# Kernel tuning notes

Measured on AMD Instinct MI355X. Metric: run time of the kernel, lower is better.

## Reference

```python
import jax, jax.numpy as jnp
import numpy as np

ENC_L, DEC_L = 4, 6
H = 8
D = 512
DFF = 2048
DLAT = 128
NTOK = 1024
NCODES = 2048
NGROUPS = 64
DG = DLAT // NGROUPS  # 2
T_ENC, BT, NSEQ = 128, 8, 16
T_DEC = 1024


def sinusoid_pe(T, d):
    pos = jnp.arange(T, dtype=jnp.float32)[:, None]
    div = jnp.exp(jnp.arange(0, d, 2, dtype=jnp.float32) * (-jnp.log(10000.0) / d))
    pe = jnp.zeros((T, d), jnp.float32)
    pe = pe.at[:, 0::2].set(jnp.sin(pos * div))
    pe = pe.at[:, 1::2].set(jnp.cos(pos * div))
    return pe[:, None, :]  # [T,1,d], seq-first broadcast over batch


def layer_norm(x, g, b):
    m = x.mean(-1, keepdims=True)
    v = ((x - m) ** 2).mean(-1, keepdims=True)
    return (x - m) * jax.lax.rsqrt(v + 1e-5) * g + b


def mha(x, Wqkv, Wo, causal):
    T, B, d = x.shape
    dh = d // H
    q, k, v = jnp.split(x @ Wqkv, 3, axis=-1)
    q = q.reshape(T, B, H, dh)
    k = k.reshape(T, B, H, dh)
    v = v.reshape(T, B, H, dh)
    scores = jnp.einsum('tbhd,sbhd->bhts', q, k) / jnp.sqrt(jnp.float32(dh))
    if causal:
        mask = jnp.tril(jnp.ones((T, T), bool))
        scores = jnp.where(mask[None, None], scores, jnp.float32(-1e9))
    attn = jax.nn.softmax(scores, axis=-1)
    out = jnp.einsum('bhts,sbhd->tbhd', attn, v).reshape(T, B, d)
    return out @ Wo


def tf_layer(x, p, i, causal):
    Wqkv, Wo, ln1g, ln1b, ln2g, ln2b, W1, b1, W2, b2 = [a[i] for a in p]
    x = layer_norm(x + mha(x, Wqkv, Wo, causal), ln1g, ln1b)
    h = jax.nn.relu(x @ W1 + b1) @ W2 + b2
    return layer_norm(x + h, ln2g, ln2b)


def forward_core(enc_inp, dec_inp, dec_inp_seq_pos, fl):
    (emb_table,
     eWqkv, eWo, eln1g, eln1b, eln2g, eln2b, eW1, eb1, eW2, eb2,
     dWqkv, dWo, dln1g, dln1b, dln2g, dln2b, dW1, db1, dW2, db2,
     W_mu, b_mu, codebook, seg_W, seg_b, W_out, b_out) = fl
    scale = jnp.sqrt(jnp.float32(D))
    # token embeddings (seq-first)
    enc_emb = emb_table[enc_inp] * scale            # [T_ENC, BT, NSEQ, D]
    dec_emb = emb_table[dec_inp] * scale            # [T_DEC, BT, D]
    x = enc_emb.reshape(T_ENC, BT * NSEQ, D) + sinusoid_pe(T_ENC, D)
    y = dec_emb + sinusoid_pe(T_DEC, D)
    enc_p = (eWqkv, eWo, eln1g, eln1b, eln2g, eln2b, eW1, eb1, eW2, eb2)
    for i in range(ENC_L):
        x = tf_layer(x, enc_p, i, False)
    mu = x[0] @ W_mu + b_mu                         # [BT*NSEQ, DLAT]
    # grouped vector quantization
    g = mu.reshape(-1, NGROUPS, DG)
    d2 = (g ** 2).sum(-1, keepdims=True) - 2.0 * jnp.einsum('bgd,cd->bgc', g, codebook) + (codebook ** 2).sum(-1)
    idx = jnp.argmin(d2, axis=-1)                   # [BT*NSEQ, NGROUPS]
    q = codebook[idx]
    sg = jax.lax.stop_gradient
    diff = jnp.mean((sg(q) - g) ** 2) + jnp.mean((q - sg(g)) ** 2)
    z = (g + sg(q - g)).reshape(-1, DLAT)           # straight-through
    # ragged scatter of per-segment latents into decoder timeline (vectorized)
    lat = z.reshape(BT, NSEQ, DLAT)
    t = jnp.arange(T_DEC)
    seg = jax.vmap(lambda p: jnp.searchsorted(p, t, side='right') - 1)(dec_inp_seq_pos)  # [BT, T_DEC]
    valid = (seg >= 0) & (seg < NSEQ)
    segc = jnp.clip(seg, 0, NSEQ - 1)
    dec_seg = jnp.where(valid[..., None], lat[jnp.arange(BT)[:, None], segc], 0.0)  # [BT, T_DEC, DLAT]
    dec_seg_emb = dec_seg.transpose(1, 0, 2)        # [T_DEC, BT, DLAT]
    # decoder with in-attention segment conditioning at every layer
    seg_proj = dec_seg_emb @ seg_W + seg_b          # [T_DEC, BT, D]
    dec_p = (dWqkv, dWo, dln1g, dln1b, dln2g, dln2b, dW1, db1, dW2, db2)
    for i in range(DEC_L):
        y = tf_layer(y + seg_proj, dec_p, i, True)
    logits = y @ W_out + b_out                      # [T_DEC, BT, NTOK]
    return mu, z, diff, logits


def setup_inputs() -> dict:
    key = jax.random.key(0)
    ks = jax.random.split(key, 16)
    rn = lambda k, shape, s=0.02: jax.random.normal(k, shape, jnp.float32) * s
    inp = {}
    inp['enc_inp'] = jax.random.randint(ks[0], (T_ENC, BT, NSEQ), 0, NTOK)
    inp['dec_inp'] = jax.random.randint(ks[1], (T_DEC, BT), 0, NTOK)
    inp['dec_inp_seq_pos'] = jnp.sort(jax.random.randint(ks[2], (BT, NSEQ + 1), 0, T_DEC), axis=-1)
    inp['emb_table'] = rn(ks[3], (NTOK, D))
    def stack(kk, L):
        sk = jax.random.split(kk, 4)
        return dict(Wqkv=rn(sk[0], (L, D, 3 * D)), Wo=rn(sk[1], (L, D, D)),
                    ln1g=jnp.ones((L, D)), ln1b=jnp.zeros((L, D)),
                    ln2g=jnp.ones((L, D)), ln2b=jnp.zeros((L, D)),
                    W1=rn(sk[2], (L, D, DFF)), b1=jnp.zeros((L, DFF)),
                    W2=rn(sk[3], (L, DFF, D)), b2=jnp.zeros((L, D)))
    for nm, v in stack(ks[4], ENC_L).items():
        inp['enc_' + nm] = v
    for nm, v in stack(ks[5], DEC_L).items():
        inp['dec_' + nm] = v
    inp['W_mu'] = rn(ks[6], (D, DLAT)); inp['b_mu'] = jnp.zeros((DLAT,))
    inp['codebook'] = rn(ks[7], (NCODES, DG), 1.0)
    inp['seg_W'] = rn(ks[8], (DLAT, D)); inp['seg_b'] = jnp.zeros((D,))
    inp['W_out'] = rn(ks[9], (D, NTOK)); inp['b_out'] = jnp.zeros((NTOK,))
    return inp


def reference(enc_inp, dec_inp, dec_inp_seq_pos, emb_table,
              enc_Wqkv, enc_Wo, enc_ln1g, enc_ln1b, enc_ln2g, enc_ln2b, enc_W1, enc_b1, enc_W2, enc_b2,
              dec_Wqkv, dec_Wo, dec_ln1g, dec_ln1b, dec_ln2g, dec_ln2b, dec_W1, dec_b1, dec_W2, dec_b2,
              W_mu, b_mu, codebook, seg_W, seg_b, W_out, b_out):
    fl = (emb_table,
          enc_Wqkv, enc_Wo, enc_ln1g, enc_ln1b, enc_ln2g, enc_ln2b, enc_W1, enc_b1, enc_W2, enc_b2,
          dec_Wqkv, dec_Wo, dec_ln1g, dec_ln1b, dec_ln2g, dec_ln2b, dec_W1, dec_b1, dec_W2, dec_b2,
          W_mu, b_mu, codebook, seg_W, seg_b, W_out, b_out)
    return forward_core(enc_inp, dec_inp, dec_inp_seq_pos, fl)
```

## Files before the change

kernel.cpp:

```cpp
#include <hip/hip_runtime.h>
#include <hip/hip_bf16.h>


using bf16 = __hip_bfloat16;

#define ENC_L 4
#define DEC_L 6
#define NH    8
#define DMODEL 512
#define DH    64
#define DFF   2048
#define DLAT  128
#define NTOK  1024
#define NCODES 2048
#define T_ENC 128
#define BT    8
#define NSEQ  16
#define T_DEC 1024
#define BENC  (BT*NSEQ)
#define EMB_SCALE 22.627416997969522f
#define LN10000 9.210340371976184f

#define ENC_CB 16
#define DEC_CB 2
// ... 153 lines not shown
                float v = ldw(W, woff + (size_t)(k0 + kk + i) * N + col0 + bn, isbf);
                unsigned short h = f2bf_rne(v);
                Bh[bn][kk + i] = h;
                Bl[bn][kk + i] = f2bf_rne(v - bf2f(h));
            }
        }
        __syncthreads();
        #pragma unroll
        for (int ks = 0; ks < 64; ks += 32) {
            short8 fah[2], fal[2], fbh[2], fbl[2];
            #pragma unroll
            for (int i = 0; i < 2; i++) {
                fah[i] = *(const short8*)&Ah[wm + i * 16 + l15][ks + quad * 8];
                fal[i] = *(const short8*)&Al[wm + i * 16 + l15][ks + quad * 8];
                fbh[i] = *(const short8*)&Bh[wn + i * 16 + l15][ks + quad * 8];
                fbl[i] = *(const short8*)&Bl[wn + i * 16 + l15][ks + quad * 8];
            }
            #pragma unroll
            for (int i = 0; i < 2; i++)
                #pragma unroll
                for (int j = 0; j < 2; j++) {
                    acc[i][j] = __builtin_amdgcn_mfma_f32_16x16x32_bf16(fah[i], fbh[j], acc[i][j], 0, 0, 0);
                    acc[i][j] = __builtin_amdgcn_mfma_f32_16x16x32_bf16(fah[i], fbl[j], acc[i][j], 0, 0, 0);
                    acc[i][j] = __builtin_amdgcn_mfma_f32_16x16x32_bf16(fal[i], fbh[j], acc[i][j], 0, 0, 0);
                }
        }
        __syncthreads();
    }
    #pragma unroll
    for (int i = 0; i < 2; i++) {
        #pragma unroll
        for (int j = 0; j < 2; j++) {
            int gc = col0 + wn + j * 16 + l15;
            float bv = bias ? ldw(bias, boff + gc, isbf) : 0.f;
            #pragma unroll
            for (int r = 0; r < 4; r++) {
                int gr = row0 + wm + i * 16 + quad * 4 + r;
                float v = acc[i][j][r] + bv;
                if (relu) v = fmaxf(v, 0.f);
                C[(size_t)gr * N + gc] = v;
            }
        }
    }
}

__global__ __launch_bounds__(256) void gemm_mfma_logits_kernel(
    const float* __restrict__ A, const void* __restrict__ W,
    const void* __restrict__ bias, float* __restrict__ C,
    int N, int K, int b0, const int* __restrict__ dflag)
{
    int isbf = dflag[0];
    __shared__ unsigned short Ah[64][LDT], Al[64][LDT];
    __shared__ unsigned short Bh[64][LDT], Bl[64][LDT];
    int tid = threadIdx.x;
    int lane = tid & 63, wave = tid >> 6;
    int quad = lane >> 4, l15 = lane & 15;
    int wm = (wave >> 1) * 32, wn = (wave & 1) * 32;
    int row0 = blockIdx.y * 64, col0 = blockIdx.x * 64;

    floatx4 acc[2][2];
    #pragma unroll
    for (int i = 0; i < 2; i++)
        #pragma unroll
        for (int j = 0; j < 2; j++)
            acc[i][j] = (floatx4){0.f, 0.f, 0.f, 0.f};

    int ar = tid >> 2;
    int ac = (tid & 3) * 4;
    int bn = tid & 63;
    int bk4 = (tid >> 6) * 4;

    for (int k0 = 0; k0 < K; k0 += 64) {
        const float* arow = A + (size_t)(row0 + ar) * K + k0;
        #pragma unroll
        for (int rep = 0; rep < 4; rep++) {
            int c = ac + rep * 16;
            floatx4 v = *(const floatx4*)(arow + c);
            #pragma unroll
            for (int i = 0; i < 4; i++) {
                unsigned short h = f2bf_rne(v[i]);
                Ah[ar][c + i] = h;
                Al[ar][c + i] = f2bf_rne(v[i] - bf2f(h));
            }
        }
        #pragma unroll
        for (int rep = 0; rep < 4; rep++) {
            int kk = bk4 + rep * 16;
            #pragma unroll
            for (int i = 0; i < 4; i++) {
                float v = ldw(W, (size_t)(k0 + kk + i) * N + col0 + bn, isbf);
                unsigned short h = f2bf_rne(v);
                Bh[bn][kk + i] = h;
                Bl[bn][kk + i] = f2bf_rne(v - bf2f(h));
            }
        }
        __syncthreads();
        #pragma unroll
        for (int ks = 0; ks < 64; ks += 32) {
            short8 fah[2], fal[2], fbh[2], fbl[2];
            #pragma unroll
            for (int i = 0; i < 2; i++) {
                fah[i] = *(const short8*)&Ah[wm + i * 16 + l15][ks + quad * 8];
                fal[i] = *(const short8*)&Al[wm + i * 16 + l15][ks + quad * 8];
                fbh[i] = *(const short8*)&Bh[wn + i * 16 + l15][ks + quad * 8];
                fbl[i] = *(const short8*)&Bl[wn + i * 16 + l15][ks + quad * 8];
            }
            #pragma unroll
            for (int i = 0; i < 2; i++)
                #pragma unroll
                for (int j = 0; j < 2; j++) {
                    acc[i][j] = __builtin_amdgcn_mfma_f32_16x16x32_bf16(fah[i], fbh[j], acc[i][j], 0, 0, 0);
                    acc[i][j] = __builtin_amdgcn_mfma_f32_16x16x32_bf16(fah[i], fbl[j], acc[i][j], 0, 0, 0);
                    acc[i][j] = __builtin_amdgcn_mfma_f32_16x16x32_bf16(fal[i], fbh[j], acc[i][j], 0, 0, 0);
                }
        }
        __syncthreads();
    }
    #pragma unroll
    for (int i = 0; i < 2; i++) {
        #pragma unroll
        for (int j = 0; j < 2; j++) {
            int gc = col0 + wn + j * 16 + l15;
            float bv = ldw(bias, gc, isbf);
            #pragma unroll
            for (int r = 0; r < 4; r++) {
                int gr = row0 + wm + i * 16 + quad * 4 + r;
                int out_row = ((gr & (T_DEC - 1)) * BT) + b0 + (gr >> 10);
                C[(size_t)out_row * N + gc] = acc[i][j][r] + bv;
            }
        }
    }
}

__global__ __launch_bounds__(256) void attn_kernel(
    const float* __restrict__ qkv, float* __restrict__ out,
    int T, int causal)
{
    __shared__ float qv[DH];
    __shared__ float sc[1024];
    __shared__ float red[256];
    __shared__ float part[256];
    int t = blockIdx.x;
    int bh = blockIdx.y;
    int bl = bh / NH, h = bh - (bh / NH) * NH;
    int tid = threadIdx.x;
    size_t row = (size_t)bl * T + t;
    const float* qp = qkv + row * (3 * DMODEL) + h * DH;
    if (tid < DH) qv[tid] = qp[tid];
    __syncthreads();
    int Tlim = causal ? (t + 1) : T;
    float lmax = -1e30f;
    for (int s = tid; s < Tlim; s += 256) {
        const float* kp = qkv + ((size_t)bl * T + s) * (3 * DMODEL) + DMODEL + h * DH;
        float dsum = 0.f;
        #pragma unroll
        for (int d = 0; d < DH; d++) dsum += qv[d] * kp[d];
        dsum *= 0.125f;
        sc[s] = dsum;
        lmax = fmaxf(lmax, dsum);
    }
    red[tid] = lmax; __syncthreads();
    for (int o = 128; o > 0; o >>= 1) {
        if (tid < o) red[tid] = fmaxf(red[tid], red[tid + o]);
        __syncthreads();
    }
    float m = red[0]; __syncthreads();
// ... 126 lines not shown
    int i = blockIdx.x * 256 + threadIdx.x;
    if (i >= n) return;
    float v = a[i] + b[i];
    c[i] = v;
    unsigned short h = f2bf_rne(v);
    ch[i] = h;
    cl[i] = f2bf_rne(v - bf2f(h));
}

__global__ void gather2_kernel(const float* __restrict__ Xc,
                               unsigned short* __restrict__ agh,
                               unsigned short* __restrict__ agl, int bj0) {
    int bl = blockIdx.x;
    int d = threadIdx.x;
    #pragma unroll
    for (int k = 0; k < 2; k++) {
        int dd = d + k * 256;
        float v = Xc[(size_t)bl * T_ENC * DMODEL + dd];
        size_t o = (size_t)(bj0 + bl) * DMODEL + dd;
        unsigned short h = f2bf_rne(v);
        agh[o] = h;
        agl[o] = f2bf_rne(v - bf2f(h));
    }
}

__global__ __launch_bounds__(128) void seg2_kernel(
    const int* __restrict__ pos, const float* __restrict__ z,
    unsigned short* __restrict__ dh, unsigned short* __restrict__ dl, int b0)
{
    int t = blockIdx.x, bl = blockIdx.y;
    int b = b0 + bl;
    __shared__ int sseg;
    if (threadIdx.x == 0) {
        int cnt = 0;
        for (int i = 0; i < NSEQ + 1; i++) cnt += (pos[b * (NSEQ + 1) + i] <= t) ? 1 : 0;
        sseg = cnt - 1;
    }
    __syncthreads();
    int seg = sseg;
    float v = 0.f;
    if (seg >= 0 && seg < NSEQ) v = z[(b * NSEQ + seg) * DLAT + threadIdx.x];
    size_t o = ((size_t)bl * T_DEC + t) * DLAT + threadIdx.x;
    unsigned short h = f2bf_rne(v);
    dh[o] = h;
    dl[o] = f2bf_rne(v - bf2f(h));
}

__global__ __launch_bounds__(256) void ln_res2_kernel(
    const float* __restrict__ a, const float* __restrict__ c,
    const float* __restrict__ g, const float* __restrict__ be, size_t goff,
    float* __restrict__ out, unsigned short* __restrict__ oh,
    unsigned short* __restrict__ ol)
{
    __shared__ float red[256];
    int row = blockIdx.x, tid = threadIdx.x;
    size_t base = (size_t)row * DMODEL;
    float x0 = a[base + tid] + c[base + tid];
    float x1 = a[base + tid + 256] + c[base + tid + 256];
    red[tid] = x0 + x1; __syncthreads();
    for (int o = 128; o > 0; o >>= 1) {
        if (tid < o) red[tid] += red[tid + o];
        __syncthreads();
    }
    float mean = red[0] * (1.f / DMODEL); __syncthreads();
    float d0 = x0 - mean, d1 = x1 - mean;
    red[tid] = d0 * d0 + d1 * d1; __syncthreads();
    for (int o = 128; o > 0; o >>= 1) {
        if (tid < o) red[tid] += red[tid + o];
        __syncthreads();
    }
    float rstd = rsqrtf(red[0] * (1.f / DMODEL) + 1e-5f);
    float o0 = d0 * rstd * g[goff + tid] + be[goff + tid];
    float o1 = d1 * rstd * g[goff + tid + 256] + be[goff + tid + 256];
    out[base + tid] = o0;
    out[base + tid + 256] = o1;
    unsigned short h0 = f2bf_rne(o0);
    oh[base + tid] = h0;
    ol[base + tid] = f2bf_rne(o0 - bf2f(h0));
    unsigned short h1 = f2bf_rne(o1);
    oh[base + tid + 256] = h1;
    ol[base + tid + 256] = f2bf_rne(o1 - bf2f(h1));
}

__global__ __launch_bounds__(256) void gemm_hl_kernel(
    const unsigned short* __restrict__ Ah, const unsigned short* __restrict__ Al,
    const unsigned short* __restrict__ Wh, const unsigned short* __restrict__ Wl,
    size_t woff, const float* __restrict__ bias, size_t boff,
    float* __restrict__ C, unsigned short* __restrict__ Ch, unsigned short* __restrict__ Cl,
    int M, int N, int K, int relu, int wmode, int b0perm)
{
    __shared__ unsigned short sAh[4096], sAl[4096], sBh[4096], sBl[4096];
    int tid = threadIdx.x;
    int lane = tid & 63, wave = tid >> 6, quad = lane >> 4, l15 = lane & 15;
    int wm = (wave >> 1) * 32, wn = (wave & 1) * 32;
    int row0 = blockIdx.y * 64, col0 = blockIdx.x * 64;
    int sr = tid >> 3, sc = (tid & 7) * 8;

    floatx4 acc[2][2];
    #pragma unroll
    for (int i = 0; i < 2; i++)
        #pragma unroll
        for (int j = 0; j < 2; j++)
            acc[i][j] = (floatx4){0.f, 0.f, 0.f, 0.f};

    const unsigned short* Wbh = Wh + woff;
    const unsigned short* Wbl = Wl + woff;

    for (int k0 = 0; k0 < K; k0 += 64) {
        #pragma unroll
        for (int rnd = 0; rnd < 2; rnd++) {
            int r = rnd * 32 + sr;
            size_t ga = (size_t)(row0 + r) * K + k0 + sc;
            size_t gb = (size_t)(col0 + r) * K + k0 + sc;
            int di = SWZ(r, sc);
            *(short8*)&sAh[di] = *(const short8*)(const void*)(Ah + ga);
            *(short8*)&sAl[di] = *(const short8*)(const void*)(Al + ga);
            *(short8*)&sBh[di] = *(const short8*)(const void*)(Wbh + gb);
            *(short8*)&sBl[di] = *(const short8*)(const void*)(Wbl + gb);
        }
        __syncthreads();
        #pragma unroll
        for (int ks = 0; ks < 64; ks += 32) {
            short8 fah[2], fal[2], fbh[2], fbl[2];
            #pragma unroll
            for (int i = 0; i < 2; i++) {
                fah[i] = *(const short8*)&sAh[SWZ(wm + i * 16 + l15, ks + quad * 8)];
                fal[i] = *(const short8*)&sAl[SWZ(wm + i * 16 + l15, ks + quad * 8)];
                fbh[i] = *(const short8*)&sBh[SWZ(wn + i * 16 + l15, ks + quad * 8)];
                fbl[i] = *(const short8*)&sBl[SWZ(wn + i * 16 + l15, ks + quad * 8)];
            }
            #pragma unroll
            for (int i = 0; i < 2; i++)
                #pragma unroll
                for (int j = 0; j < 2; j++) {
                    acc[i][j] = __builtin_amdgcn_mfma_f32_16x16x32_bf16(fah[i], fbh[j], acc[i][j], 0, 0, 0);
                    acc[i][j] = __builtin_amdgcn_mfma_f32_16x16x32_bf16(fal[i], fbh[j], acc[i][j], 0, 0, 0);
                    acc[i][j] = __builtin_amdgcn_mfma_f32_16x16x32_bf16(fah[i], fbl[j], acc[i][j], 0, 0, 0);
                }
        }
        __syncthreads();
    }
    #pragma unroll
    for (int i = 0; i < 2; i++) {
        #pragma unroll
        for (int j = 0; j < 2; j++) {
            int gc = col0 + wn + j * 16 + l15;
            float bv = bias ? bias[boff + gc] : 0.f;
            #pragma unroll
            for (int r = 0; r < 4; r++) {
                int gr = row0 + wm + i * 16 + quad * 4 + r;
                float v = acc[i][j][r] + bv;
                if (relu) v = fmaxf(v, 0.f);
                size_t orow = (size_t)gr;
                if (b0perm >= 0) orow = (size_t)((gr & (T_DEC - 1)) * BT + b0perm + (gr >> 10));
                if (wmode & 1) C[orow * N + gc] = v;
                if (wmode & 2) {
                    unsigned short hh = f2bf_rne(v);
                    Ch[(size_t)gr * N + gc] = hh;
                    Cl[(size_t)gr * N + gc] = f2bf_rne(v - bf2f(hh));
                }
            }
        }
    }
}

__global__ __launch_bounds__(256) void qkv_prep_kernel(
    const float* __restrict__ QKV,
    unsigned short* __restrict__ Qh, unsigned short* __restrict__ Ql,
    unsigned short* __restrict__ Kh, unsigned short* __restrict__ Kl,
    unsigned short* __restrict__ VhT, unsigned short* __restrict__ VlT, int T)
{
    int tid = threadIdx.x;
    int r0 = blockIdx.x * 64;
    int ct = blockIdx.y;
    int sr = tid >> 3, sc = (tid & 7) * 8;
    if (ct < 16) {
        int c0 = ct * 64;
        #pragma unroll
        for (int rnd = 0; rnd < 2; rnd++) {
            int r = r0 + rnd * 32 + sr;
            const float* src = QKV + (size_t)r * 1536 + c0 + sc;
            short8 hv, lv;
            #pragma unroll
            for (int i = 0; i < 8; i++) {
                float v = src[i];
                unsigned short h = f2bf_rne(v);
                hv[i] = (short)h;
                lv[i] = (short)f2bf_rne(v - bf2f(h));
            }
            int col = c0 + sc;
            if (col < 512) {
                size_t o = (size_t)r * 512 + col;
                *(short8*)&Qh[o] = hv;
                *(short8*)&Ql[o] = lv;
            } else {
                size_t o = (size_t)r * 512 + col - 512;
                *(short8*)&Kh[o] = hv;
                *(short8*)&Kl[o] = lv;
            }
        }
    } else {
        __shared__ unsigned short th[64][72], tl[64][72];
        int vc0 = (ct - 16) * 64;
        #pragma unroll
        for (int rnd = 0; rnd < 2; rnd++) {
            int rr = rnd * 32 + sr;
            const float* src = QKV + (size_t)(r0 + rr) * 1536 + 1024 + vc0 + sc;
            #pragma unroll
            for (int i = 0; i < 8; i++) {
                float v = src[i];
                unsigned short h = f2bf_rne(v);
                th[rr][sc + i] = h;
                tl[rr][sc + i] = f2bf_rne(v - bf2f(h));
            }
        }
        __syncthreads();
        int bl = r0 / T;
        int t0 = r0 - bl * T;
        #pragma unroll
        for (int rnd = 0; rnd < 2; rnd++) {
            int dr = rnd * 32 + sr;
            int gd = vc0 + dr;
            int hh = gd >> 6, dd = gd & 63;
            size_t obase = ((size_t)(bl * NH + hh) * 64 + dd) * T + t0 + sc;
            short8 hv, lv;
            #pragma unroll
            for (int i = 0; i < 8; i++) {
                hv[i] = (short)th[sc + i][dr];
                lv[i] = (short)tl[sc + i][dr];
            }
            *(short8*)&VhT[obase] = hv;
            *(short8*)&VlT[obase] = lv;
        }
// ... 211 lines not shown
        in_sizes[10] == 4194304 && in_sizes[14] == 4718592 && in_sizes[15] == 1572864 &&
        in_sizes[24] == 65536 && in_sizes[25] == 128 && in_sizes[26] == 4096 &&
        in_sizes[29] == 524288 && in_sizes[30] == 1024;
    if (!order_ok) {
        fill_kernel<<<64, 256, 0, stream>>>(out_mu, 100.0f, 16384);
        return;
    }

    char* cur = (char*)d_ws;
    auto alloc = [&](size_t bytes) -> void* {
        void* p = (void*)cur;
        cur += (bytes + 255) & ~(size_t)255;
        return p;
    };
    float* XC   = (float*)alloc((size_t)MC * 512 * 4);
    unsigned short* XCh = (unsigned short*)alloc((size_t)MC * 512 * 2);
    unsigned short* XCl = (unsigned short*)alloc((size_t)MC * 512 * 2);
    float* SPC  = (float*)alloc((size_t)MC * 512 * 4);
    float* TIN  = (float*)alloc((size_t)MC * 512 * 4);
    unsigned short* TINh = (unsigned short*)alloc((size_t)MC * 512 * 2);
    unsigned short* TINl = (unsigned short*)alloc((size_t)MC * 512 * 2);
    float* QKV  = (float*)alloc((size_t)MC * 1536 * 4);
    unsigned short* Qh = (unsigned short*)alloc((size_t)MC * 512 * 2);
    unsigned short* Ql = (unsigned short*)alloc((size_t)MC * 512 * 2);
    unsigned short* Kh = (unsigned short*)alloc((size_t)MC * 512 * 2);
    unsigned short* Kl = (unsigned short*)alloc((size_t)MC * 512 * 2);
    unsigned short* VhT = (unsigned short*)alloc((size_t)MC * 512 * 2);
    unsigned short* VlT = (unsigned short*)alloc((size_t)MC * 512 * 2);
    unsigned short* AOh = (unsigned short*)alloc((size_t)MC * 512 * 2);
    unsigned short* AOl = (unsigned short*)alloc((size_t)MC * 512 * 2);
    float* Pb   = (float*)alloc((size_t)MC * 512 * 4);
    unsigned short* Hh = (unsigned short*)alloc((size_t)MC * 2048 * 2);
    unsigned short* Hl = (unsigned short*)alloc((size_t)MC * 2048 * 2);
    unsigned short* DSCh = (unsigned short*)alloc((size_t)MC * 128 * 2);
    unsigned short* DSCl = (unsigned short*)alloc((size_t)MC * 128 * 2);
    unsigned short* AGh = (unsigned short*)alloc((size_t)128 * 512 * 2);
    unsigned short* AGl = (unsigned short*)alloc((size_t)128 * 512 * 2);
    float* MU   = (float*)alloc((size_t)128 * 128 * 4);
    float* Z    = (float*)alloc((size_t)128 * 128 * 4);
    float* ACC  = (float*)alloc(256);
    int*   FLG  = (int*)alloc(256);
    float* VECS = (float*)alloc(VEC_TOTAL * 4);
    unsigned short* WH = (unsigned short*)alloc(W_TOTAL * 2);
    unsigned short* WL = (unsigned short*)alloc(W_TOTAL * 2);
    size_t need_new = (size_t)(cur - (char*)d_ws);

    if (ws_size >= need_new) {
        detect_kernel<<<1, 64, 0, stream>>>((const unsigned int*)eln1g, FLG, ACC);

        conv_w_kernel<<<dim3(1536/32, 512/32, 4), 256, 0, stream>>>(eWqkv, WH+OFF_EWQKV, WL+OFF_EWQKV, 512, 1536, FLG);
        conv_w_kernel<<<dim3( 512/32, 512/32, 4), 256, 0, stream>>>(eWo,   WH+OFF_EWO,   WL+OFF_EWO,   512,  512, FLG);
        conv_w_kernel<<<dim3(2048/32, 512/32, 4), 256, 0, stream>>>(eW1,   WH+OFF_EW1,   WL+OFF_EW1,   512, 2048, FLG);
        conv_w_kernel<<<dim3( 512/32,2048/32, 4), 256, 0, stream>>>(eW2,   WH+OFF_EW2,   WL+OFF_EW2,  2048,  512, FLG);
        conv_w_kernel<<<dim3(1536/32, 512/32, 6), 256, 0, stream>>>(dWqkv, WH+OFF_DWQKV, WL+OFF_DWQKV, 512, 1536, FLG);
        conv_w_kernel<<<dim3( 512/32, 512/32, 6), 256, 0, stream>>>(dWo,   WH+OFF_DWO,   WL+OFF_DWO,   512,  512, FLG);
        conv_w_kernel<<<dim3(2048/32, 512/32, 6), 256, 0, stream>>>(dW1,   WH+OFF_DW1,   WL+OFF_DW1,   512, 2048, FLG);
        conv_w_kernel<<<dim3( 512/32,2048/32, 6), 256, 0, stream>>>(dW2,   WH+OFF_DW2,   WL+OFF_DW2,  2048,  512, FLG);
        conv_w_kernel<<<dim3( 128/32, 512/32, 1), 256, 0, stream>>>(W_mu,  WH+OFF_WMU,   WL+OFF_WMU,   512,  128, FLG);
        conv_w_kernel<<<dim3( 512/32, 128/32, 1), 256, 0, stream>>>(seg_W, WH+OFF_SEGW,  WL+OFF_SEGW,  128,  512, FLG);
        conv_w_kernel<<<dim3(1024/32, 512/32, 1), 256, 0, stream>>>(W_out, WH+OFF_WOUT,  WL+OFF_WOUT,  512, 1024, FLG);

        conv_vec_kernel<<<8, 256, 0, stream>>>(eln1g, VECS+VELN1G, 2048, FLG);
        conv_vec_kernel<<<8, 256, 0, stream>>>(eln1b, VECS+VELN1B, 2048, FLG);
        conv_vec_kernel<<<8, 256, 0, stream>>>(eln2g, VECS+VELN2G, 2048, FLG);
        conv_vec_kernel<<<8, 256, 0, stream>>>(eln2b, VECS+VELN2B, 2048, FLG);
        conv_vec_kernel<<<12, 256, 0, stream>>>(dln1g, VECS+VDLN1G, 3072, FLG);
        conv_vec_kernel<<<12, 256, 0, stream>>>(dln1b, VECS+VDLN1B, 3072, FLG);
        conv_vec_kernel<<<12, 256, 0, stream>>>(dln2g, VECS+VDLN2G, 3072, FLG);
        conv_vec_kernel<<<12, 256, 0, stream>>>(dln2b, VECS+VDLN2B, 3072, FLG);
        conv_vec_kernel<<<32, 256, 0, stream>>>(eb1, VECS+VEB1, 8192, FLG);
        conv_vec_kernel<<<8, 256, 0, stream>>>(eb2, VECS+VEB2, 2048, FLG);
        conv_vec_kernel<<<48, 256, 0, stream>>>(db1, VECS+VDB1, 12288, FLG);
        conv_vec_kernel<<<12, 256, 0, stream>>>(db2, VECS+VDB2, 3072, FLG);
        conv_vec_kernel<<<1, 256, 0, stream>>>(b_mu, VECS+VBMU, 128, FLG);
        conv_vec_kernel<<<2, 256, 0, stream>>>(seg_b, VECS+VSEGB, 512, FLG);
        conv_vec_kernel<<<4, 256, 0, stream>>>(b_out, VECS+VBOUT, 1024, FLG);

        for (int c = 0; c < BENC / ENC_CB; c++) {
            int bj0 = c * ENC_CB;
            embed2_kernel<<<4096, 256, 0, stream>>>(enc_inp, emb, XC, XCh, XCl, T_ENC, BENC, bj0, FLG);
            for (int i = 0; i < ENC_L; i++) {
                size_t oQ = (size_t)i * 512 * 1536, oO = (size_t)i * 512 * 512;
                size_t o1 = (size_t)i * 512 * 2048, o2 = (size_t)i * 2048 * 512;
                gemm_hl_kernel<<<dim3(24, 32), 256, 0, stream>>>(
                    XCh, XCl, WH+OFF_EWQKV, WL+OFF_EWQKV, oQ, nullptr, 0,
                    QKV, nullptr, nullptr, MC, 1536, 512, 0, 1, -1);
                qkv_prep_kernel<<<dim3(32, 24), 256, 0, stream>>>(QKV, Qh, Ql, Kh, Kl, VhT, VlT, T_ENC);
                attn_flash_kernel<<<dim3(T_ENC/64, ENC_CB*NH), 256, 0, stream>>>(
                    Qh, Ql, Kh, Kl, VhT, VlT, AOh, AOl, T_ENC, 0);
                gemm_hl_kernel<<<dim3(8, 32), 256, 0, stream>>>(
                    AOh, AOl, WH+OFF_EWO, WL+OFF_EWO, oO, nullptr, 0,
                    Pb, nullptr, nullptr, MC, 512, 512, 0, 1, -1);
                ln_res2_kernel<<<MC, 256, 0, stream>>>(XC, Pb, VECS+VELN1G, VECS+VELN1B,
                    (size_t)i*512, XC, XCh, XCl);
                gemm_hl_kernel<<<dim3(32, 32), 256, 0, stream>>>(
                    XCh, XCl, WH+OFF_EW1, WL+OFF_EW1, o1, VECS+VEB1, (size_t)i*2048,
                    nullptr, Hh, Hl, MC, 2048, 512, 1, 2, -1);
                gemm_hl_kernel<<<dim3(8, 32), 256, 0, stream>>>(
                    Hh, Hl, WH+OFF_EW2, WL+OFF_EW2, o2, VECS+VEB2, (size_t)i*512,
                    Pb, nullptr, nullptr, MC, 512, 2048, 0, 1, -1);
                ln_res2_kernel<<<MC, 256, 0, stream>>>(XC, Pb, VECS+VELN2G, VECS+VELN2B,
                    (size_t)i*512, XC, XCh, XCl);
            }
            gather2_kernel<<<ENC_CB, 256, 0, stream>>>(XC, AGh, AGl, bj0);
        }

        gemm_hl_kernel<<<dim3(2, 2), 256, 0, stream>>>(
            AGh, AGl, WH+OFF_WMU, WL+OFF_WMU, 0, VECS+VBMU, 0,
            MU, nullptr, nullptr, BENC, 128, 512, 0, 1, -1);
        vq_kernel<<<BENC, 64, 0, stream>>>(MU, cbk, Z, ACC, FLG);
        copy_kernel<<<64, 256, 0, stream>>>(MU, out_mu, 16384);
        copy_kernel<<<64, 256, 0, stream>>>(Z, out_z, 16384);
        diff_kernel<<<1, 1, 0, stream>>>(ACC, out_diff);

        for (int c = 0; c < BT / DEC_CB; c++) {
            int b0 = c * DEC_CB;
            seg2_kernel<<<dim3(T_DEC, DEC_CB), 128, 0, stream>>>(seq_pos, Z, DSCh, DSCl, b0);
            gemm_hl_kernel<<<dim3(8, 32), 256, 0, stream>>>(
                DSCh, DSCl, WH+OFF_SEGW, WL+OFF_SEGW, 0, VECS+VSEGB, 0,
                SPC, nullptr, nullptr, MC, 512, 128, 0, 1, -1);
            embed2_kernel<<<4096, 256, 0, stream>>>(dec_inp, emb, XC, XCh, XCl, T_DEC, BT, b0, FLG);
            for (int i = 0; i < DEC_L; i++) {
                size_t oQ = (size_t)i * 512 * 1536, oO = (size_t)i * 512 * 512;
                size_t o1 = (size_t)i * 512 * 2048, o2 = (size_t)i * 2048 * 512;
                add2_kernel<<<4096, 256, 0, stream>>>(XC, SPC, TIN, TINh, TINl, MC * 512);
                gemm_hl_kernel<<<dim3(24, 32), 256, 0, stream>>>(
                    TINh, TINl, WH+OFF_DWQKV, WL+OFF_DWQKV, oQ, nullptr, 0,
                    QKV, nullptr, nullptr, MC, 1536, 512, 0, 1, -1);
                qkv_prep_kernel<<<dim3(32, 24), 256, 0, stream>>>(QKV, Qh, Ql, Kh, Kl, VhT, VlT, T_DEC);
                attn_flash_kernel<<<dim3(T_DEC/64, DEC_CB*NH), 256, 0, stream>>>(
                    Qh, Ql, Kh, Kl, VhT, VlT, AOh, AOl, T_DEC, 1);
                gemm_hl_kernel<<<dim3(8, 32), 256, 0, stream>>>(
                    AOh, AOl, WH+OFF_DWO, WL+OFF_DWO, oO, nullptr, 0,
                    Pb, nullptr, nullptr, MC, 512, 512, 0, 1, -1);
                ln_res2_kernel<<<MC, 256, 0, stream>>>(TIN, Pb, VECS+VDLN1G, VECS+VDLN1B,
                    (size_t)i*512, TIN, TINh, TINl);
                gemm_hl_kernel<<<dim3(32, 32), 256, 0, stream>>>(
                    TINh, TINl, WH+OFF_DW1, WL+OFF_DW1, o1, VECS+VDB1, (size_t)i*2048,
                    nullptr, Hh, Hl, MC, 2048, 512, 1, 2, -1);
                gemm_hl_kernel<<<dim3(8, 32), 256, 0, stream>>>(
                    Hh, Hl, WH+OFF_DW2, WL+OFF_DW2, o2, VECS+VDB2, (size_t)i*512,
                    Pb, nullptr, nullptr, MC, 512, 2048, 0, 1, -1);
                ln_res2_kernel<<<MC, 256, 0, stream>>>(TIN, Pb, VECS+VDLN2G, VECS+VDLN2B,
                    (size_t)i*512, XC, XCh, XCl);
            }
            gemm_hl_kernel<<<dim3(16, 32), 256, 0, stream>>>(
                XCh, XCl, WH+OFF_WOUT, WL+OFF_WOUT, 0, VECS+VBOUT, 0,
                out_logits, nullptr, nullptr, MC, 1024, 512, 0, 1, b0);
        }
        return;
    }

    float* ws  = (float*)d_ws;
    float* oXC  = ws;
    float* oSPC = ws + 1048576;
    float* oTIN = ws + 2097152;
    float* oQKV = ws + 3145728;
    float* oAO  = ws + 6291456;
    float* oH   = ws + 3145728;
    float* oP   = ws + 7340032;
    float* oDSC = ws + 8388608;
    float* oAG  = ws + 8650752;
    float* oMU  = ws + 8716288;
    float* oZ   = ws + 8732672;
    float* oACC = ws + 8749056;
    int*   oFLG = (int*)(ws + 8749057);

    detect_kernel<<<1, 64, 0, stream>>>((const unsigned int*)eln1g, oFLG, oACC);

    for (int c = 0; c < BENC / ENC_CB; c++) {
        int bj0 = c * ENC_CB;
        embed_kernel<<<(MC * DMODEL + 255) / 256, 256, 0, stream>>>(
            enc_inp, emb, oXC, T_ENC, BENC, bj0, ENC_CB, oFLG);
        for (int i = 0; i < ENC_L; i++) {
            size_t oQ  = (size_t)i * DMODEL * 3 * DMODEL;
            size_t oO  = (size_t)i * DMODEL * DMODEL;
            size_t o1  = (size_t)i * DMODEL * DFF;
            size_t o2  = (size_t)i * DFF * DMODEL;
            size_t oLn = (size_t)i * DMODEL;
            size_t oB1 = (size_t)i * DFF;
            gemm_mfma_kernel<<<dim3(3 * DMODEL / 64, MC / 64), 256, 0, stream>>>(
                oXC, eWqkv, oQ, nullptr, 0, oQKV, MC, 3 * DMODEL, DMODEL, 0, oFLG);
            attn_kernel<<<dim3(T_ENC, ENC_CB * NH), 256, 0, stream>>>(oQKV, oAO, T_ENC, 0);
            gemm_mfma_kernel<<<dim3(DMODEL / 64, MC / 64), 256, 0, stream>>>(
                oAO, eWo, oO, nullptr, 0, oP, MC, DMODEL, DMODEL, 0, oFLG);
            ln_res_kernel<<<MC, 256, 0, stream>>>(oXC, oP, eln1g, eln1b, oLn, oXC, oFLG);
            gemm_mfma_kernel<<<dim3(DFF / 64, MC / 64), 256, 0, stream>>>(
                oXC, eW1, o1, eb1, oB1, oH, MC, DFF, DMODEL, 1, oFLG);
            gemm_mfma_kernel<<<dim3(DMODEL / 64, MC / 64), 256, 0, stream>>>(
                oH, eW2, o2, eb2, oLn, oP, MC, DMODEL, DFF, 0, oFLG);
            ln_res_kernel<<<MC, 256, 0, stream>>>(oXC, oP, eln2g, eln2b, oLn, oXC, oFLG);
        }
        gather_t0_kernel<<<ENC_CB, 256, 0, stream>>>(oXC, oAG, bj0);
    }

    gemm_mfma_kernel<<<dim3(DLAT / 64, BENC / 64), 256, 0, stream>>>(
        oAG, W_mu, 0, b_mu, 0, oMU, BENC, DLAT, DMODEL, 0, oFLG);
    vq_kernel<<<BENC, 64, 0, stream>>>(oMU, cbk, oZ, oACC, oFLG);
    copy_kernel<<<64, 256, 0, stream>>>(oMU, out_mu, 16384);
    copy_kernel<<<64, 256, 0, stream>>>(oZ, out_z, 16384);
    diff_kernel<<<1, 1, 0, stream>>>(oACC, out_diff);

    for (int c = 0; c < BT / DEC_CB; c++) {
        int b0 = c * DEC_CB;
        seg_kernel<<<dim3(T_DEC, DEC_CB), 128, 0, stream>>>(seq_pos, oZ, oDSC, b0);
        gemm_mfma_kernel<<<dim3(DMODEL / 64, MC / 64), 256, 0, stream>>>(
            oDSC, seg_W, 0, seg_b, 0, oSPC, MC, DMODEL, DLAT, 0, oFLG);
        embed_kernel<<<(MC * DMODEL + 255) / 256, 256, 0, stream>>>(
            dec_inp, emb, oXC, T_DEC, BT, b0, DEC_CB, oFLG);
        for (int i = 0; i < DEC_L; i++) {
            size_t oQ  = (size_t)i * DMODEL * 3 * DMODEL;
            size_t oO  = (size_t)i * DMODEL * DMODEL;
            size_t o1  = (size_t)i * DMODEL * DFF;
            size_t o2  = (size_t)i * DFF * DMODEL;
            size_t oLn = (size_t)i * DMODEL;
            size_t oB1 = (size_t)i * DFF;
            add_kernel<<<(MC * DMODEL + 255) / 256, 256, 0, stream>>>(oXC, oSPC, oTIN, MC * DMODEL);
            gemm_mfma_kernel<<<dim3(3 * DMODEL / 64, MC / 64), 256, 0, stream>>>(
                oTIN, dWqkv, oQ, nullptr, 0, oQKV, MC, 3 * DMODEL, DMODEL, 0, oFLG);
            attn_kernel<<<dim3(T_DEC, DEC_CB * NH), 256, 0, stream>>>(oQKV, oAO, T_DEC, 1);
            gemm_mfma_kernel<<<dim3(DMODEL / 64, MC / 64), 256, 0, stream>>>(
                oAO, dWo, oO, nullptr, 0, oP, MC, DMODEL, DMODEL, 0, oFLG);
            ln_res_kernel<<<MC, 256, 0, stream>>>(oTIN, oP, dln1g, dln1b, oLn, oTIN, oFLG);
            gemm_mfma_kernel<<<dim3(DFF / 64, MC / 64), 256, 0, stream>>>(
                oTIN, dW1, o1, db1, oB1, oH, MC, DFF, DMODEL, 1, oFLG);
            gemm_mfma_kernel<<<dim3(DMODEL / 64, MC / 64), 256, 0, stream>>>(
                oH, dW2, o2, db2, oLn, oP, MC, DMODEL, DFF, 0, oFLG);
            ln_res_kernel<<<MC, 256, 0, stream>>>(oTIN, oP, dln2g, dln2b, oLn, oXC, oFLG);
        }
        gemm_mfma_logits_kernel<<<dim3(NTOK / 64, MC / 64), 256, 0, stream>>>(
            oXC, W_out, b_out, out_logits, NTOK, DMODEL, b0, oFLG);
// ... 3 lines not shown
```

Baseline: 7.633 ms.

## Replace LDS-tiled split-bf16 GEMM with single-wave direct-load kernel, skip low weight term

Replaces the 256-thread shared-memory tiled GEMM with a 64-thread, one-wave kernel. Each wave computes a full 64x64 tile with a 4x4 accumulator grid and loads MFMA fragments straight from global memory, with no LDS staging and no barriers. When the data flag says the weights are bf16, the weight low part is taken as zero and its MFMA is skipped, cutting the GEMM work from three products to two. The trade-off is less latency hiding and less data reuse per block, possibly uncoalesced 16-byte fragment loads, and higher register pressure. A stray empty loop is also added to another kernel.

Result: slower. 13.59 ms (+78.0%).

```diff
diff --git a/kernel.cpp b/kernel.cpp
--- a/kernel.cpp
+++ b/kernel.cpp
@@ -259,6 +259,10 @@
                 Ah[ar][c + i] = h;
                 Al[ar][c + i] = f2bf_rne(v[i] - bf2f(h));
             }
+        }
+        #pragma unroll
+        for (int rep = 0; rep < 4; rep++) {
+            int kk = bk4 + rep * 4;
         }
         #pragma unroll
         for (int rep = 0; rep < 4; rep++) {
@@ -551,73 +555,80 @@
     ol[base + tid + 256] = f2bf_rne(o1 - bf2f(h1));
 }
 
-__global__ __launch_bounds__(256) void gemm_hl_kernel(
+__global__ __launch_bounds__(64) void gemm_dx_kernel(
     const unsigned short* __restrict__ Ah, const unsigned short* __restrict__ Al,
     const unsigned short* __restrict__ Wh, const unsigned short* __restrict__ Wl,
     size_t woff, const float* __restrict__ bias, size_t boff,
     float* __restrict__ C, unsigned short* __restrict__ Ch, unsigned short* __restrict__ Cl,
-    int M, int N, int K, int relu, int wmode, int b0perm)
-{
-    __shared__ unsigned short sAh[4096], sAl[4096], sBh[4096], sBl[4096];
-    int tid = threadIdx.x;
-    int lane = tid & 63, wave = tid >> 6, quad = lane >> 4, l15 = lane & 15;
-    int wm = (wave >> 1) * 32, wn = (wave & 1) * 32;
+    int M, int N, int K, int relu, int wmode, int b0perm, const int* __restrict__ dflag)
+{
+    int isbf = dflag[0];
+    int lane = threadIdx.x;
+    int quad = lane >> 4, l15 = lane & 15;
     int row0 = blockIdx.y * 64, col0 = blockIdx.x * 64;
-    int sr = tid >> 3, sc = (tid & 7) * 8;
-
-    floatx4 acc[2][2];
-    #pragma unroll
-    for (int i = 0; i < 2; i++)
-        #pragma unroll
-        for (int j = 0; j < 2; j++)
+
+    floatx4 acc[4][4];
+    #pragma unroll
+    for (int i = 0; i < 4; i++)
+        #pragma unroll
+        for (int j = 0; j < 4; j++)
             acc[i][j] = (floatx4){0.f, 0.f, 0.f, 0.f};
 
-    const unsigned short* Wbh = Wh + woff;
-    const unsigned short* Wbl = Wl + woff;
-
-    for (int k0 = 0; k0 < K; k0 += 64) {
-        #pragma unroll
-        for (int rnd = 0; rnd < 2; rnd++) {
-            int r = rnd * 32 + sr;
-            size_t ga = (size_t)(row0 + r) * K + k0 + sc;
-            size_t gb = (size_t)(col0 + r) * K + k0 + sc;
-            int di = SWZ(r, sc);
-            *(short8*)&sAh[di] = *(const short8*)(const void*)(Ah + ga);
-            *(short8*)&sAl[di] = *(const short8*)(const void*)(Al + ga);
-            *(short8*)&sBh[di] = *(const short8*)(const void*)(Wbh + gb);
-            *(short8*)&sBl[di] = *(const short8*)(const void*)(Wbl + gb);
-        }
-        __syncthreads();
-        #pragma unroll
-        for (int ks = 0; ks < 64; ks += 32) {
-            short8 fah[2], fal[2], fbh[2], fbl[2];
-            #pragma unroll
-            for (int i = 0; i < 2; i++) {
-                fah[i] = *(const short8*)&sAh[SWZ(wm + i * 16 + l15, ks + quad * 8)];
-                fal[i] = *(const short8*)&sAl[SWZ(wm + i * 16 + l15, ks + quad * 8)];
-                fbh[i] = *(const short8*)&sBh[SWZ(wn + i * 16 + l15, ks + quad * 8)];
-                fbl[i] = *(const short8*)&sBl[SWZ(wn + i * 16 + l15, ks + quad * 8)];
-            }
-            #pragma unroll
-            for (int i = 0; i < 2; i++)
+    const unsigned short* ah = Ah + (size_t)(row0 + l15) * K + quad * 8;
+    const unsigned short* al = Al + (size_t)(row0 + l15) * K + quad * 8;
+    const unsigned short* bh = Wh + woff + (size_t)(col0 + l15) * K + quad * 8;
+    const unsigned short* bl = Wl + woff + (size_t)(col0 + l15) * K + quad * 8;
+    const size_t fstep = (size_t)16 * K;
+
+    if (isbf) {
+        for (int k0 = 0; k0 < K; k0 += 32) {
+            short8 fa[4], fl4[4];
+            #pragma unroll
+            for (int i = 0; i < 4; i++) {
+                fa[i]  = *(const short8*)(const void*)(ah + i * fstep + k0);
+                fl4[i] = *(const short8*)(const void*)(al + i * fstep + k0);
+            }
+            #pragma unroll
+            for (int j = 0; j < 4; j++) {
+                short8 fb = *(const short8*)(const void*)(bh + j * fstep + k0);
                 #pragma unroll
-                for (int j = 0; j < 2; j++) {
-                    acc[i][j] = __builtin_amdgcn_mfma_f32_16x16x32_bf16(fah[i], fbh[j], acc[i][j], 0, 0, 0);
-                    acc[i][j] = __builtin_amdgcn_mfma_f32_16x16x32_bf16(fal[i], fbh[j], acc[i][j], 0, 0, 0);
-                    acc[i][j] = __builtin_amdgcn_mfma_f32_16x16x32_bf16(fah[i], fbl[j], acc[i][j], 0, 0, 0);
+                for (int i = 0; i < 4; i++) {
+                    acc[i][j] = __builtin_amdgcn_mfma_f32_16x16x32_bf16(fa[i], fb, acc[i][j], 0, 0, 0);
+                    acc[i][j] = __builtin_amdgcn_mfma_f32_16x16x32_bf16(fl4[i], fb, acc[i][j], 0, 0, 0);
                 }
-        }
-        __syncthreads();
-    }
-    #pragma unroll
-    for (int i = 0; i < 2; i++) {
-        #pragma unroll
-        for (int j = 0; j < 2; j++) {
-            int gc = col0 + wn + j * 16 + l15;
+            }
+        }
+    } else {
+        for (int k0 = 0; k0 < K; k0 += 32) {
+            short8 fa[4], fl4[4];
+            #pragma unroll
+            for (int i = 0; i < 4; i++) {
+                fa[i]  = *(const short8*)(const void*)(ah + i * fstep + k0);
+                fl4[i] = *(const short8*)(const void*)(al + i * fstep + k0);
+            }
+            #pragma unroll
+            for (int j = 0; j < 4; j++) {
+                short8 fb  = *(const short8*)(const void*)(bh + j * fstep + k0);
+                short8 fbl = *(const short8*)(const void*)(bl + j * fstep + k0);
+                #pragma unroll
+                for (int i = 0; i < 4; i++) {
+                    acc[i][j] = __builtin_amdgcn_mfma_f32_16x16x32_bf16(fa[i], fb, acc[i][j], 0, 0, 0);
+                    acc[i][j] = __builtin_amdgcn_mfma_f32_16x16x32_bf16(fl4[i], fb, acc[i][j], 0, 0, 0);
+                    acc[i][j] = __builtin_amdgcn_mfma_f32_16x16x32_bf16(fa[i], fbl, acc[i][j], 0, 0, 0);
+                }
+            }
+        }
+    }
+
+    #pragma unroll
+    for (int i = 0; i < 4; i++) {
+        #pragma unroll
+        for (int j = 0; j < 4; j++) {
+            int gc = col0 + j * 16 + l15;
             float bv = bias ? bias[boff + gc] : 0.f;
             #pragma unroll
             for (int r = 0; r < 4; r++) {
-                int gr = row0 + wm + i * 16 + quad * 4 + r;
+                int gr = row0 + i * 16 + quad * 4 + r;
                 float v = acc[i][j][r] + bv;
                 if (relu) v = fmaxf(v, 0.f);
                 size_t orow = (size_t)gr;
@@ -995,32 +1006,32 @@
             for (int i = 0; i < ENC_L; i++) {
                 size_t oQ = (size_t)i * 512 * 1536, oO = (size_t)i * 512 * 512;
                 size_t o1 = (size_t)i * 512 * 2048, o2 = (size_t)i * 2048 * 512;
-                gemm_hl_kernel<<<dim3(24, 32), 256, 0, stream>>>(
+                gemm_dx_kernel<<<dim3(24, 32), 64, 0, stream>>>(
                     XCh, XCl, WH+OFF_EWQKV, WL+OFF_EWQKV, oQ, nullptr, 0,
-                    QKV, nullptr, nullptr, MC, 1536, 512, 0, 1, -1);
+                    QKV, nullptr, nullptr, MC, 1536, 512, 0, 1, -1, FLG);
                 qkv_prep_kernel<<<dim3(32, 24), 256, 0, stream>>>(QKV, Qh, Ql, Kh, Kl, VhT, VlT, T_ENC);
                 attn_flash_kernel<<<dim3(T_ENC/64, ENC_CB*NH), 256, 0, stream>>>(
                     Qh, Ql, Kh, Kl, VhT, VlT, AOh, AOl, T_ENC, 0);
-                gemm_hl_kernel<<<dim3(8, 32), 256, 0, stream>>>(
+                gemm_dx_kernel<<<dim3(8, 32), 64, 0, stream>>>(
                     AOh, AOl, WH+OFF_EWO, WL+OFF_EWO, oO, nullptr, 0,
-                    Pb, nullptr, nullptr, MC, 512, 512, 0, 1, -1);
+                    Pb, nullptr, nullptr, MC, 512, 512, 0, 1, -1, FLG);
                 ln_res2_kernel<<<MC, 256, 0, stream>>>(XC, Pb, VECS+VELN1G, VECS+VELN1B,
                     (size_t)i*512, XC, XCh, XCl);
-                gemm_hl_kernel<<<dim3(32, 32), 256, 0, stream>>>(
+                gemm_dx_kernel<<<dim3(32, 32), 64, 0, stream>>>(
                     XCh, XCl, WH+OFF_EW1, WL+OFF_EW1, o1, VECS+VEB1, (size_t)i*2048,
-                    nullptr, Hh, Hl, MC, 2048, 512, 1, 2, -1);
-                gemm_hl_kernel<<<dim3(8, 32), 256, 0, stream>>>(
+                    nullptr, Hh, Hl, MC, 2048, 512, 1, 2, -1, FLG);
+                gemm_dx_kernel<<<dim3(8, 32), 64, 0, stream>>>(
                     Hh, Hl, WH+OFF_EW2, WL+OFF_EW2, o2, VECS+VEB2, (size_t)i*512,
-                    Pb, nullptr, nullptr, MC, 512, 2048, 0, 1, -1);
+                    Pb, nullptr, nullptr, MC, 512, 2048, 0, 1, -1, FLG);
                 ln_res2_kernel<<<MC, 256, 0, stream>>>(XC, Pb, VECS+VELN2G, VECS+VELN2B,
                     (size_t)i*512, XC, XCh, XCl);
             }
             gather2_kernel<<<ENC_CB, 256, 0, stream>>>(XC, AGh, AGl, bj0);
         }
 
-        gemm_hl_kernel<<<dim3(2, 2), 256, 0, stream>>>(
+        gemm_dx_kernel<<<dim3(2, 2), 64, 0, stream>>>(
             AGh, AGl, WH+OFF_WMU, WL+OFF_WMU, 0, VECS+VBMU, 0,
-            MU, nullptr, nullptr, BENC, 128, 512, 0, 1, -1);
+            MU, nullptr, nullptr, BENC, 128, 512, 0, 1, -1, FLG);
         vq_kernel<<<BENC, 64, 0, stream>>>(MU, cbk, Z, ACC, FLG);
         copy_kernel<<<64, 256, 0, stream>>>(MU, out_mu, 16384);
         copy_kernel<<<64, 256, 0, stream>>>(Z, out_z, 16384);
@@ -1029,37 +1040,37 @@
         for (int c = 0; c < BT / DEC_CB; c++) {
             int b0 = c * DEC_CB;
             seg2_kernel<<<dim3(T_DEC, DEC_CB), 128, 0, stream>>>(seq_pos, Z, DSCh, DSCl, b0);
-            gemm_hl_kernel<<<dim3(8, 32), 256, 0, stream>>>(
+            gemm_dx_kernel<<<dim3(8, 32), 64, 0, stream>>>(
                 DSCh, DSCl, WH+OFF_SEGW, WL+OFF_SEGW, 0, VECS+VSEGB, 0,
-                SPC, nullptr, nullptr, MC, 512, 128, 0, 1, -1);
+                SPC, nullptr, nullptr, MC, 512, 128, 0, 1, -1, FLG);
             embed2_kernel<<<4096, 256, 0, stream>>>(dec_inp, emb, XC, XCh, XCl, T_DEC, BT, b0, FLG);
             for (int i = 0; i < DEC_L; i++) {
                 size_t oQ = (size_t)i * 512 * 1536, oO = (size_t)i * 512 * 512;
                 size_t o1 = (size_t)i * 512 * 2048, o2 = (size_t)i * 2048 * 512;
                 add2_kernel<<<4096, 256, 0, stream>>>(XC, SPC, TIN, TINh, TINl, MC * 512);
-                gemm_hl_kernel<<<dim3(24, 32), 256, 0, stream>>>(
+                gemm_dx_kernel<<<dim3(24, 32), 64, 0, stream>>>(
                     TINh, TINl, WH+OFF_DWQKV, WL+OFF_DWQKV, oQ, nullptr, 0,
-                    QKV, nullptr, nullptr, MC, 1536, 512, 0, 1, -1);
+                    QKV, nullptr, nullptr, MC, 1536, 512, 0, 1, -1, FLG);
                 qkv_prep_kernel<<<dim3(32, 24), 256, 0, stream>>>(QKV, Qh, Ql, Kh, Kl, VhT, VlT, T_DEC);
                 attn_flash_kernel<<<dim3(T_DEC/64, DEC_CB*NH), 256, 0, stream>>>(
                     Qh, Ql, Kh, Kl, VhT, VlT, AOh, AOl, T_DEC, 1);
-                gemm_hl_kernel<<<dim3(8, 32), 256, 0, stream>>>(
+                gemm_dx_kernel<<<dim3(8, 32), 64, 0, stream>>>(
                     AOh, AOl, WH+OFF_DWO, WL+OFF_DWO, oO, nullptr, 0,
-                    Pb, nullptr, nullptr, MC, 512, 512, 0, 1, -1);
+                    Pb, nullptr, nullptr, MC, 512, 512, 0, 1, -1, FLG);
                 ln_res2_kernel<<<MC, 256, 0, stream>>>(TIN, Pb, VECS+VDLN1G, VECS+VDLN1B,
                     (size_t)i*512, TIN, TINh, TINl);
-                gemm_hl_kernel<<<dim3(32, 32), 256, 0, stream>>>(
+                gemm_dx_kernel<<<dim3(32, 32), 64, 0, stream>>>(
                     TINh, TINl, WH+OFF_DW1, WL+OFF_DW1, o1, VECS+VDB1, (size_t)i*2048,
-                    nullptr, Hh, Hl, MC, 2048, 512, 1, 2, -1);
-                gemm_hl_kernel<<<dim3(8, 32), 256, 0, stream>>>(
+                    nullptr, Hh, Hl, MC, 2048, 512, 1, 2, -1, FLG);
+                gemm_dx_kernel<<<dim3(8, 32), 64, 0, stream>>>(
                     Hh, Hl, WH+OFF_DW2, WL+OFF_DW2, o2, VECS+VDB2, (size_t)i*512,
-                    Pb, nullptr, nullptr, MC, 512, 2048, 0, 1, -1);
+                    Pb, nullptr, nullptr, MC, 512, 2048, 0, 1, -1, FLG);
                 ln_res2_kernel<<<MC, 256, 0, stream>>>(TIN, Pb, VECS+VDLN2G, VECS+VDLN2B,
                     (size_t)i*512, XC, XCh, XCl);
             }
-            gemm_hl_kernel<<<dim3(16, 32), 256, 0, stream>>>(
+            gemm_dx_kernel<<<dim3(16, 32), 64, 0, stream>>>(
                 XCh, XCl, WH+OFF_WOUT, WL+OFF_WOUT, 0, VECS+VBOUT, 0,
-                out_logits, nullptr, nullptr, MC, 1024, 512, 0, 1, b0);
+                out_logits, nullptr, nullptr, MC, 1024, 512, 0, 1, b0, FLG);
         }
         return;
     }
```
